# Kernel optimization log

Measured on AMD Instinct MI355X. Metric: run time of the kernel, lower is better.

## Reference

```python
import jax, jax.numpy as jnp
import numpy as np

EMBED_DIM = 768
N_HEADS = 12
HEAD_DIM = EMBED_DIM // N_HEADS
SCALE = HEAD_DIM ** 0.5


def setup_inputs() -> dict:
    key = jax.random.key(0)
    k1, k2, k3 = jax.random.split(key, 3)
    x = jax.random.normal(k1, (2, 2048, EMBED_DIM), dtype=jnp.float32)
    # weights stored [in, out] so forward is x @ W (equivalent to torch Linear with W.T)
    w_qkv = jax.random.normal(k2, (EMBED_DIM, 3 * EMBED_DIM), dtype=jnp.float32) * (EMBED_DIM ** -0.5)
    w_proj = jax.random.normal(k3, (EMBED_DIM, EMBED_DIM), dtype=jnp.float32) * (EMBED_DIM ** -0.5)
    return {"x": x, "w_qkv": w_qkv, "w_proj": w_proj}


def reference(x, w_qkv, w_proj):
    B, N, C = x.shape
    qkv = x @ w_qkv  # [B, N, 3C]
    qkv = qkv.reshape(B, N, 3, N_HEADS, HEAD_DIM)
    qkv = jnp.transpose(qkv, (2, 0, 3, 1, 4))  # [3, B, H, N, hd]
    q, k, v = qkv[0], qkv[1], qkv[2]
    attn = jnp.einsum("bhnd,bhmd->bhnm", q, k) / SCALE  # [B, H, N, N]
    attn = jax.nn.softmax(attn, axis=-1)
    out = jnp.einsum("bhnm,bhmd->bhnd", attn, v)  # [B, H, N, hd]
    out = jnp.transpose(out, (0, 2, 1, 3)).reshape(B, N, C)
    return out @ w_proj
```

## Files before the change

kernel.cpp:

```cpp
#include <hip/hip_runtime.h>
#include <hip/hip_bf16.h>
#include <stdint.h>

typedef uint16_t u16;
typedef __attribute__((ext_vector_type(4))) float f32x4;
typedef __attribute__((ext_vector_type(8))) short bf16x8;

#define LOG2E 1.4426950408889634f

static __device__ __forceinline__ u16 f2b(float x){
  union { float f; uint32_t u; } a; a.f = x;
  uint32_t r = a.u + 0x7FFFu + ((a.u >> 16) & 1u);
  return (u16)(r >> 16);
}

static __device__ __forceinline__ uint32_t pkrhu(float lo, float hi){
  union { float f; uint32_t u; } a, b; a.f = lo; b.f = hi;
  return __builtin_amdgcn_perm(b.u + 0x8000u, a.u + 0x8000u, 0x07060302u);
}

#define GLD16(g, l) __builtin_amdgcn_global_load_lds((const __attribute__((address_space(1))) void*)(g), (__attribute__((address_space(3))) void*)(l), 16, 0, 0)

__global__ __launch_bounds__(256) void k_prep(const float* __restrict__ x, u16* __restrict__ Xb,
                                              const float* __restrict__ wqkv, u16* __restrict__ WqkvT,
                                              const float* __restrict__ wproj, u16* __restrict__ WprojT){
  __shared__ float t[32][33];
  const int bid = blockIdx.x, tid = threadIdx.x;
  if (bid < 1536){
    int i = bid * 256 + tid;
    const f32x4* p = (const f32x4*)(x + (size_t)i * 8);
    f32x4 a = p[0], b = p[1];
    u16 h[8];
#pragma unroll
    for (int j = 0; j < 4; ++j){ h[j] = f2b(a[j]); h[4+j] = f2b(b[j]); }
    *(bf16x8*)(Xb + (size_t)i * 8) = *(const bf16x8*)h;
    return;
  }
  const float* in; u16* out; int R, C, bx, by;
  if (bid < 1536 + 1728){
    int q = bid - 1536; in = wqkv; out = WqkvT; R = 768; C = 2304; bx = q % 72; by = q / 72;
  } else {
    int q = bid - 1536 - 1728; in = wproj; out = WprojT; R = 768; C = 768; bx = q % 24; by = q / 24;
  }
  int c0 = bx * 32, r0 = by * 32;
  int tx = tid & 31, ty = tid >> 5;
#pragma unroll
  for (int i = 0; i < 32; i += 8) t[ty + i][tx] = in[(size_t)(r0 + ty + i) * C + c0 + tx];
  __syncthreads();
#pragma unroll
  for (int i = 0; i < 32; i += 8) out[(size_t)(c0 + ty + i) * R + r0 + tx] = f2b(t[tx][ty + i]);
}

__global__ __launch_bounds__(256) void k_gemmqkv(const u16* __restrict__ A, const u16* __restrict__ Bt,
                                                 u16* __restrict__ Qp, u16* __restrict__ Kp, u16* __restrict__ Vtp){
  __shared__ __align__(16) u16 SM[14336];
  u16* Al = SM; u16* Bl = SM + 8192;
  const int tid = threadIdx.x;
  const int w = tid >> 6, l = tid & 63;
  const int m0 = blockIdx.x * 128, n0 = blockIdx.y * 96;
  const int wm = (w >> 1) * 64, wn = (w & 1) * 48;
  const int lg = l >> 4, lr = l & 15;
  f32x4 acc[4][3] = {};
  const u16* asrc = A  + (size_t)(m0 + w*32 + (l >> 3)) * 768 + (l & 7) * 8;
  const u16* bsrc = Bt + (size_t)(n0 + w*24 + (l >> 3)) * 768 + (l & 7) * 8;
  for (int k0 = 0; k0 < 768; k0 += 64){
#pragma unroll
    for (int i = 0; i < 4; ++i)
      GLD16(asrc + (size_t)(i*8)*768 + k0, &Al[(w*32 + i*8) * 64]);
#pragma unroll
    for (int i = 0; i < 3; ++i)
      GLD16(bsrc + (size_t)(i*8)*768 + k0, &Bl[(w*24 + i*8) * 64]);
    __syncthreads();
    bf16x8 af[4][2], bfr[3][2];
#pragma unroll
    for (int mf = 0; mf < 4; ++mf)
#pragma unroll
      for (int ks = 0; ks < 2; ++ks)
        af[mf][ks] = *(const bf16x8*)&Al[(wm + mf*16 + lr) * 64 + ks*32 + lg*8];
#pragma unroll
    for (int nf = 0; nf < 3; ++nf)
#pragma unroll
      for (int ks = 0; ks < 2; ++ks)
        bfr[nf][ks] = *(const bf16x8*)&Bl[(wn + nf*16 + lr) * 64 + ks*32 + lg*8];
#pragma unroll
    for (int ks = 0; ks < 2; ++ks)
#pragma unroll
      for (int mf = 0; mf < 4; ++mf)
#pragma unroll
        for (int nf = 0; nf < 3; ++nf)
          acc[mf][nf] = __builtin_amdgcn_mfma_f32_16x16x32_bf16(af[mf][ks], bfr[nf][ks], acc[mf][nf], 0, 0, 0);
    __syncthreads();
  }

  const int which = n0 / 768;
  const int nl0 = n0 - which * 768;
  if (which < 2){
    u16* dst = (which == 0) ? Qp : Kp;
    const float sc = (which == 0) ? 0.125f * LOG2E : 1.0f;
#pragma unroll
    for (int mf = 0; mf < 4; ++mf)
#pragma unroll
      for (int nf = 0; nf < 3; ++nf)
#pragma unroll
        for (int r = 0; r < 4; ++r){
          int m = m0 + wm + mf*16 + lg*4 + r;
          int n = nl0 + wn + nf*16 + lr;
          int b = m >> 11, row = m & 2047, hh = n >> 6, d = n & 63;
          dst[(size_t)((b*12 + hh)*2048 + row) * 64 + d] = f2b(acc[mf][nf][r] * sc);
        }
  } else {
#pragma unroll
    for (int mf = 0; mf < 4; ++mf)
#pragma unroll
      for (int nf = 0; nf < 3; ++nf)
#pragma unroll
        for (int r = 0; r < 4; ++r){
          int mrow = wm + mf*16 + lg*4 + r;
          int c    = wn + nf*16 + lr;
          SM[c * 128 + mrow] = f2b(acc[mf][nf][r]);
        }
    __syncthreads();
#pragma unroll
    for (int rr = 0; rr < 6; ++rr){
      int c  = rr*16 + (tid >> 4);
      int mo = (tid & 15) * 8;
      bf16x8 v = *(const bf16x8*)&SM[c * 128 + mo];
      int n = nl0 + c, hh = n >> 6, d = n & 63;
      int m = m0 + mo, b = m >> 11, key = m & 2047;
      *(bf16x8*)&Vtp[(size_t)((b*12 + hh)*64 + d) * 2048 + key] = v;
    }
  }
}

__global__ __launch_bounds__(256) void k_gemm64(const u16* __restrict__ A, const u16* __restrict__ Bt,
                                                float* __restrict__ Co){
  __shared__ __align__(16) u16 SM[8192];
  u16* Al = SM; u16* Bl = SM + 4096;
  const int tid = threadIdx.x;
  const int w = tid >> 6, l = tid & 63;
  const int m0 = blockIdx.x * 64, n0 = blockIdx.y * 64;
  const int wm = (w >> 1) * 32, wn = (w & 1) * 32;
  const int lg = l >> 4, lr = l & 15;
  f32x4 acc[2][2] = {};
  const u16* asrc = A  + (size_t)(m0 + w*16 + (l >> 3)) * 768 + (l & 7) * 8;
  const u16* bsrc = Bt + (size_t)(n0 + w*16 + (l >> 3)) * 768 + (l & 7) * 8;
  for (int k0 = 0; k0 < 768; k0 += 64){
#pragma unroll
    for (int i = 0; i < 2; ++i){
      GLD16(asrc + (size_t)(i*8)*768 + k0, &Al[(w*16 + i*8) * 64]);
      GLD16(bsrc + (size_t)(i*8)*768 + k0, &Bl[(w*16 + i*8) * 64]);
    }
    __syncthreads();
    bf16x8 af[2][2], bfr[2][2];
#pragma unroll
    for (int mf = 0; mf < 2; ++mf)
#pragma unroll
      for (int ks = 0; ks < 2; ++ks){
        af[mf][ks]  = *(const bf16x8*)&Al[(wm + mf*16 + lr) * 64 + ks*32 + lg*8];
        bfr[mf][ks] = *(const bf16x8*)&Bl[(wn + mf*16 + lr) * 64 + ks*32 + lg*8];
      }
#pragma unroll
    for (int ks = 0; ks < 2; ++ks)
#pragma unroll
      for (int mf = 0; mf < 2; ++mf)
#pragma unroll
        for (int nf = 0; nf < 2; ++nf)
          acc[mf][nf] = __builtin_amdgcn_mfma_f32_16x16x32_bf16(af[mf][ks], bfr[nf][ks], acc[mf][nf], 0, 0, 0);
    __syncthreads();
  }
#pragma unroll
  for (int mf = 0; mf < 2; ++mf)
#pragma unroll
    for (int nf = 0; nf < 2; ++nf)
#pragma unroll
      for (int r = 0; r < 4; ++r)
        Co[(size_t)(m0 + wm + mf*16 + lg*4 + r) * 768 + n0 + wn + nf*16 + lr] = acc[mf][nf][r];
}

__global__ __launch_bounds__(256) void k_attn(const u16* __restrict__ Qp, const u16* __restrict__ Kp,
                                              const u16* __restrict__ Vtp, u16* __restrict__ AO){
  __shared__ __align__(16) u16 SM[24576];
  const int tid = threadIdx.x, w = tid >> 6, l = tid & 63;
  const int qh = w >> 1, kh = w & 1;
  const int lg = l >> 4, lr = l & 15;
  const int qt_b = blockIdx.x, bh = blockIdx.y;
  const int b = bh / 12, hh = bh - b * 12;
  const size_t base = (size_t)bh * (2048 * 64);
  const u16* Qg = Qp + base; const u16* Kg = Kp + base; const u16* Vg = Vtp + base;
  const int q0w = qt_b * 64 + qh * 32;
  const int rsw = (lr & 7) * 8;

  bf16x8 qf[2][2];
#pragma unroll
  for (int qt = 0; qt < 2; ++qt)
#pragma unroll
    for (int ks = 0; ks < 2; ++ks)
      qf[qt][ks] = *(const bf16x8*)&Qg[(size_t)(q0w + qt*16 + lr) * 64 + ks*32 + lg*8];

  f32x4 oacc[2][4] = {};
  float lp[2] = {0.f, 0.f};

  const int pl0 = w*8 + (l >> 3);
  const int sk0 = 8*((pl0 >> 2) & 3) + 4*((pl0 >> 4) & 1) + (pl0 & 3);
  const int csw = (((l & 7) ^ ((l >> 3) & 7)) << 3);
  const u16* kLp = Kg + (size_t)sk0 * 64 + csw;
  const u16* kUp = kLp + 32 * 64;
  const u16* vLp = Vg + ((size_t)pl0 << 11) + csw;
  const u16* vUp = vLp + ((size_t)32 << 11);
  const int dlo = (w*8) * 64, dhi = (w*8 + 32) * 64;
  u16* const K0lo = SM + 0     + dlo;  u16* const K0hi = SM + 0     + dhi;
  u16* const K1lo = SM + 4096  + dlo;  u16* const K1hi = SM + 4096  + dhi;
  u16* const K2lo = SM + 8192  + dlo;  u16* const K2hi = SM + 8192  + dhi;
  u16* const V0lo = SM + 12288 + dlo;  u16* const V0hi = SM + 12288 + dhi;
  u16* const V1lo = SM + 16384 + dlo;  u16* const V1hi = SM + 16384 + dhi;
  u16* const V2lo = SM + 20480 + dlo;  u16* const V2hi = SM + 20480 + dhi;

  auto compute = [&](const u16* Kc, const u16* Vc){
    f32x4 s[2][2] = {};
    bf16x8 kfr[2][2];
#pragma unroll
    for (int kf = 0; kf < 2; ++kf)
#pragma unroll
      for (int ks = 0; ks < 2; ++ks)
        kfr[kf][ks] = *(const bf16x8*)&Kc[(kh*32 + kf*16 + lr) * 64 + ((ks*32 + lg*8) ^ rsw)];
    __builtin_amdgcn_s_setprio(1);
#pragma unroll
    for (int ks = 0; ks < 2; ++ks)
#pragma unroll
      for (int kf = 0; kf < 2; ++kf)
#pragma unroll
        for (int qt = 0; qt < 2; ++qt)
          s[qt][kf] = __builtin_amdgcn_mfma_f32_16x16x32_bf16(kfr[kf][ks], qf[qt][ks], s[qt][kf], 0, 0, 0);
    __builtin_amdgcn_s_setprio(0);

    bf16x8 pa[2];
#pragma unroll
    for (int qt = 0; qt < 2; ++qt){
      float p00 = __builtin_exp2f(s[qt][0][0]);
      float p01 = __builtin_exp2f(s[qt][0][1]);
      float p02 = __builtin_exp2f(s[qt][0][2]);
      float p03 = __builtin_exp2f(s[qt][0][3]);
      float p10 = __builtin_exp2f(s[qt][1][0]);
      float p11 = __builtin_exp2f(s[qt][1][1]);
      float p12 = __builtin_exp2f(s[qt][1][2]);
      float p13 = __builtin_exp2f(s[qt][1][3]);
      lp[qt] += ((p00 + p01) + (p02 + p03)) + ((p10 + p11) + (p12 + p13));
      union { uint32_t u[4]; bf16x8 v; } fr;
      fr.u[0] = pkrhu(p00, p01);
      fr.u[1] = pkrhu(p02, p03);
      fr.u[2] = pkrhu(p10, p11);
      fr.u[3] = pkrhu(p12, p13);
      pa[qt] = fr.v;
    }

    bf16x8 vfr[4];
#pragma unroll
    for (int nf = 0; nf < 4; ++nf)
      vfr[nf] = *(const bf16x8*)&Vc[(nf*16 + lr) * 64 + ((kh*32 + lg*8) ^ rsw)];
    __builtin_amdgcn_s_setprio(1);
#pragma unroll
    for (int qt = 0; qt < 2; ++qt)
#pragma unroll
      for (int nf = 0; nf < 4; ++nf)
        oacc[qt][nf] = __builtin_amdgcn_mfma_f32_16x16x32_bf16(vfr[nf], pa[qt], oacc[qt][nf], 0, 0, 0);
    __builtin_amdgcn_s_setprio(0);
  };

#define STAGE4(KL, KH, VL, VH) do { GLD16(kLp, KL); GLD16(kUp, KH); GLD16(vLp, VL); GLD16(vUp, VH); \
                                    kLp += 4096; kUp += 4096; vLp += 64; vUp += 64; } while(0)
#define BAR_CNT8  do { asm volatile("s_waitcnt vmcnt(8)" ::: "memory"); \
                       __builtin_amdgcn_s_barrier(); __builtin_amdgcn_sched_barrier(0); } while(0)
#define BAR_CNT0  do { asm volatile("s_waitcnt vmcnt(0)" ::: "memory"); \
                       __builtin_amdgcn_s_barrier(); __builtin_amdgcn_sched_barrier(0); } while(0)

  STAGE4(K0lo, K0hi, V0lo, V0hi);
  STAGE4(K1lo, K1hi, V1lo, V1hi);
  BAR_CNT8;

  for (int g = 0; g < 10; ++g){
    STAGE4(K2lo, K2hi, V2lo, V2hi);
    compute(SM + 0,     SM + 12288);
    BAR_CNT8;
    STAGE4(K0lo, K0hi, V0lo, V0hi);
    compute(SM + 4096,  SM + 16384);
    BAR_CNT8;
    STAGE4(K1lo, K1hi, V1lo, V1hi);
    compute(SM + 8192,  SM + 20480);
    BAR_CNT8;
  }
  compute(SM + 0,    SM + 12288);
  BAR_CNT0;
  compute(SM + 4096, SM + 16384);

#undef STAGE4
#undef BAR_CNT8
#undef BAR_CNT0

  float lt[2];
#pragma unroll
  for (int qt = 0; qt < 2; ++qt){
    float t = lp[qt];
    t += __shfl_xor(t, 16);
    t += __shfl_xor(t, 32);
    lt[qt] = t;
  }

  __syncthreads();
  float* Osc = (float*)SM;
  float* Lsc = Osc + 64 * 65;
  if (kh == 1){
#pragma unroll
    for (int qt = 0; qt < 2; ++qt)
#pragma unroll
      for (int nf = 0; nf < 4; ++nf)
#pragma unroll
        for (int r = 0; r < 4; ++r)
          Osc[(qh*32 + qt*16 + lr) * 65 + nf*16 + lg*4 + r] = oacc[qt][nf][r];
    if (lg == 0){
      Lsc[qh*32 + lr]      = lt[0];
      Lsc[qh*32 + 16 + lr] = lt[1];
    }
  }
  __syncthreads();
  if (kh == 0){
#pragma unroll
    for (int qt = 0; qt < 2; ++qt){
      float inv = 1.0f / (lt[qt] + Lsc[qh*32 + qt*16 + lr]);
#pragma unroll
      for (int nf = 0; nf < 4; ++nf)
#pragma unroll
        for (int r = 0; r < 4; ++r){
          float o = oacc[qt][nf][r] + Osc[(qh*32 + qt*16 + lr) * 65 + nf*16 + lg*4 + r];
          AO[(size_t)((b << 11) + q0w + qt*16 + lr) * 768 + hh*64 + nf*16 + lg*4 + r] = f2b(o * inv);
        }
    }
  }
}

extern "C" void kernel_launch(void* const* d_in, const int* in_sizes, int n_in,
                              void* d_out, int out_size, void* d_ws, size_t ws_size,
                              hipStream_t stream){
  const float* x      = (const float*)d_in[0];
  const float* w_qkv  = (const float*)d_in[1];
  const float* w_proj = (const float*)d_in[2];
  float* out = (float*)d_out;
  char* ws = (char*)d_ws;
  u16* Xb     = (u16*)(ws + 0);
  u16* WqkvT  = (u16*)(ws + 6291456);
  u16* WprojT = (u16*)(ws + 9830400);
  u16* Qp     = (u16*)(ws + 11010048);
  u16* Kp     = (u16*)(ws + 17301504);
  u16* Vtp    = (u16*)(ws + 23592960);
  u16* AO     = (u16*)(ws + 29884416);

  k_prep<<<3840, 256, 0, stream>>>(x, Xb, w_qkv, WqkvT, w_proj, WprojT);
  k_gemmqkv<<<dim3(32, 24), 256, 0, stream>>>(Xb, WqkvT, Qp, Kp, Vtp);
  k_attn<<<dim3(32, 24), 256, 0, stream>>>(Qp, Kp, Vtp, AO);
  k_gemm64<<<dim3(64, 12), 256, 0, stream>>>(AO, WprojT, out);
}
```

Baseline: 91.41 us.

## Double attention block to 512 threads with 16-row query tiles per wave

The attention kernel now runs 8 waves per block instead of 4, and each wave owns a 16-row query tile instead of two, which halves per-wave accumulator state. The 64-key tile loads are spread across all 512 threads with two async LDS loads each, and the wait count is adjusted to match. Launch bounds request 6 blocks per CU. The aim is more waves in flight to hide latency, paid for with less reuse of each K/V fragment read from LDS per MFMA, since every K/V fragment is now read by twice as many waves.

```diff
diff --git a/kernel.cpp b/kernel.cpp
--- a/kernel.cpp
+++ b/kernel.cpp
@@ -177,163 +177,128 @@
         Co[(size_t)(m0 + wm + mf*16 + lg*4 + r) * 768 + n0 + wn + nf*16 + lr] = acc[mf][nf][r];
 }
 
-__global__ __launch_bounds__(256) void k_attn(const u16* __restrict__ Qp, const u16* __restrict__ Kp,
-                                              const u16* __restrict__ Vtp, u16* __restrict__ AO){
+__global__ __launch_bounds__(512, 6) void k_attn(const u16* __restrict__ Qp, const u16* __restrict__ Kp,
+                                                 const u16* __restrict__ Vtp, u16* __restrict__ AO){
   __shared__ __align__(16) u16 SM[24576];
   const int tid = threadIdx.x, w = tid >> 6, l = tid & 63;
-  const int qh = w >> 1, kh = w & 1;
+  const int qh = w >> 2, kh = (w >> 1) & 1;
+  const int QH = w >> 1, KH = w & 1;
   const int lg = l >> 4, lr = l & 15;
   const int qt_b = blockIdx.x, bh = blockIdx.y;
   const int b = bh / 12, hh = bh - b * 12;
   const size_t base = (size_t)bh * (2048 * 64);
   const u16* Qg = Qp + base; const u16* Kg = Kp + base; const u16* Vg = Vtp + base;
-  const int q0w = qt_b * 64 + qh * 32;
+  const int q0w = qt_b * 64 + QH * 16;
   const int rsw = (lr & 7) * 8;
 
-  bf16x8 qf[2][2];
-#pragma unroll
-  for (int qt = 0; qt < 2; ++qt)
+  bf16x8 qf[2];
+#pragma unroll
+  for (int ks = 0; ks < 2; ++ks)
+    qf[ks] = *(const bf16x8*)&Qg[(size_t)(q0w + lr) * 64 + ks*32 + lg*8];
+
+  f32x4 oacc[4] = {};
+  float lp = 0.f;
+
+  const int p_  = tid >> 3;
+  const int sk  = 32*(p_ >> 5) + 8*((p_ >> 2) & 3) + 4*((p_ >> 4) & 1) + (p_ & 3);
+  const int cs8 = (((tid & 7) ^ (p_ & 7)) << 3);
+  const u16* kp = Kg + (size_t)sk * 64 + cs8;
+  const u16* vp = Vg + ((size_t)p_ << 11) + cs8;
+  const int drow = p_ * 64;
+  u16* const K0 = SM + 0     + drow;  u16* const V0 = SM + 12288 + drow;
+  u16* const K1 = SM + 4096  + drow;  u16* const V1 = SM + 16384 + drow;
+  u16* const K2 = SM + 8192  + drow;  u16* const V2 = SM + 20480 + drow;
+
+  auto compute = [&](const u16* Kc, const u16* Vc){
+    f32x4 s[2] = {};
+    bf16x8 kfr[2][2];
+#pragma unroll
+    for (int kf = 0; kf < 2; ++kf)
+#pragma unroll
+      for (int ks = 0; ks < 2; ++ks)
+        kfr[kf][ks] = *(const bf16x8*)&Kc[(KH*32 + kf*16 + lr) * 64 + ((ks*32 + lg*8) ^ rsw)];
+    __builtin_amdgcn_s_setprio(1);
 #pragma unroll
     for (int ks = 0; ks < 2; ++ks)
-      qf[qt][ks] = *(const bf16x8*)&Qg[(size_t)(q0w + qt*16 + lr) * 64 + ks*32 + lg*8];
-
-  f32x4 oacc[2][4] = {};
-  float lp[2] = {0.f, 0.f};
-
-  const int pl0 = w*8 + (l >> 3);
-  const int sk0 = 8*((pl0 >> 2) & 3) + 4*((pl0 >> 4) & 1) + (pl0 & 3);
-  const int csw = (((l & 7) ^ ((l >> 3) & 7)) << 3);
-  const u16* kLp = Kg + (size_t)sk0 * 64 + csw;
-  const u16* kUp = kLp + 32 * 64;
-  const u16* vLp = Vg + ((size_t)pl0 << 11) + csw;
-  const u16* vUp = vLp + ((size_t)32 << 11);
-  const int dlo = (w*8) * 64, dhi = (w*8 + 32) * 64;
-  u16* const K0lo = SM + 0     + dlo;  u16* const K0hi = SM + 0     + dhi;
-  u16* const K1lo = SM + 4096  + dlo;  u16* const K1hi = SM + 4096  + dhi;
-  u16* const K2lo = SM + 8192  + dlo;  u16* const K2hi = SM + 8192  + dhi;
-  u16* const V0lo = SM + 12288 + dlo;  u16* const V0hi = SM + 12288 + dhi;
-  u16* const V1lo = SM + 16384 + dlo;  u16* const V1hi = SM + 16384 + dhi;
-  u16* const V2lo = SM + 20480 + dlo;  u16* const V2hi = SM + 20480 + dhi;
-
-  auto compute = [&](const u16* Kc, const u16* Vc){
-    f32x4 s[2][2] = {};
-    bf16x8 kfr[2][2];
-#pragma unroll
-    for (int kf = 0; kf < 2; ++kf)
-#pragma unroll
-      for (int ks = 0; ks < 2; ++ks)
-        kfr[kf][ks] = *(const bf16x8*)&Kc[(kh*32 + kf*16 + lr) * 64 + ((ks*32 + lg*8) ^ rsw)];
+#pragma unroll
+      for (int kf = 0; kf < 2; ++kf)
+        s[kf] = __builtin_amdgcn_mfma_f32_16x16x32_bf16(kfr[kf][ks], qf[ks], s[kf], 0, 0, 0);
+    __builtin_amdgcn_s_setprio(0);
+
+    float p00 = __builtin_exp2f(s[0][0]);
+    float p01 = __builtin_exp2f(s[0][1]);
+    float p02 = __builtin_exp2f(s[0][2]);
+    float p03 = __builtin_exp2f(s[0][3]);
+    float p10 = __builtin_exp2f(s[1][0]);
+    float p11 = __builtin_exp2f(s[1][1]);
+    float p12 = __builtin_exp2f(s[1][2]);
+    float p13 = __builtin_exp2f(s[1][3]);
+    lp += ((p00 + p01) + (p02 + p03)) + ((p10 + p11) + (p12 + p13));
+    union { uint32_t u[4]; bf16x8 v; } fr;
+    fr.u[0] = pkrhu(p00, p01);
+    fr.u[1] = pkrhu(p02, p03);
+    fr.u[2] = pkrhu(p10, p11);
+    fr.u[3] = pkrhu(p12, p13);
+
+    bf16x8 vfr[4];
+#pragma unroll
+    for (int nf = 0; nf < 4; ++nf)
+      vfr[nf] = *(const bf16x8*)&Vc[(nf*16 + lr) * 64 + ((KH*32 + lg*8) ^ rsw)];
     __builtin_amdgcn_s_setprio(1);
 #pragma unroll
-    for (int ks = 0; ks < 2; ++ks)
-#pragma unroll
-      for (int kf = 0; kf < 2; ++kf)
-#pragma unroll
-        for (int qt = 0; qt < 2; ++qt)
-          s[qt][kf] = __builtin_amdgcn_mfma_f32_16x16x32_bf16(kfr[kf][ks], qf[qt][ks], s[qt][kf], 0, 0, 0);
-    __builtin_amdgcn_s_setprio(0);
-
-    bf16x8 pa[2];
-#pragma unroll
-    for (int qt = 0; qt < 2; ++qt){
-      float p00 = __builtin_exp2f(s[qt][0][0]);
-      float p01 = __builtin_exp2f(s[qt][0][1]);
-      float p02 = __builtin_exp2f(s[qt][0][2]);
-      float p03 = __builtin_exp2f(s[qt][0][3]);
-      float p10 = __builtin_exp2f(s[qt][1][0]);
-      float p11 = __builtin_exp2f(s[qt][1][1]);
-      float p12 = __builtin_exp2f(s[qt][1][2]);
-      float p13 = __builtin_exp2f(s[qt][1][3]);
-      lp[qt] += ((p00 + p01) + (p02 + p03)) + ((p10 + p11) + (p12 + p13));
-      union { uint32_t u[4]; bf16x8 v; } fr;
-      fr.u[0] = pkrhu(p00, p01);
-      fr.u[1] = pkrhu(p02, p03);
-      fr.u[2] = pkrhu(p10, p11);
-      fr.u[3] = pkrhu(p12, p13);
-      pa[qt] = fr.v;
-    }
-
-    bf16x8 vfr[4];
-#pragma unroll
     for (int nf = 0; nf < 4; ++nf)
-      vfr[nf] = *(const bf16x8*)&Vc[(nf*16 + lr) * 64 + ((kh*32 + lg*8) ^ rsw)];
-    __builtin_amdgcn_s_setprio(1);
-#pragma unroll
-    for (int qt = 0; qt < 2; ++qt)
-#pragma unroll
-      for (int nf = 0; nf < 4; ++nf)
-        oacc[qt][nf] = __builtin_amdgcn_mfma_f32_16x16x32_bf16(vfr[nf], pa[qt], oacc[qt][nf], 0, 0, 0);
+      oacc[nf] = __builtin_amdgcn_mfma_f32_16x16x32_bf16(vfr[nf], fr.v, oacc[nf], 0, 0, 0);
     __builtin_amdgcn_s_setprio(0);
   };
 
-#define STAGE4(KL, KH, VL, VH) do { GLD16(kLp, KL); GLD16(kUp, KH); GLD16(vLp, VL); GLD16(vUp, VH); \
-                                    kLp += 4096; kUp += 4096; vLp += 64; vUp += 64; } while(0)
-#define BAR_CNT8  do { asm volatile("s_waitcnt vmcnt(8)" ::: "memory"); \
+#define STAGE2(KD, VD) do { GLD16(kp, KD); GLD16(vp, VD); kp += 4096; vp += 64; } while(0)
+#define BAR_CNT2  do { asm volatile("s_waitcnt vmcnt(2)" ::: "memory"); \
                        __builtin_amdgcn_s_barrier(); __builtin_amdgcn_sched_barrier(0); } while(0)
 #define BAR_CNT0  do { asm volatile("s_waitcnt vmcnt(0)" ::: "memory"); \
                        __builtin_amdgcn_s_barrier(); __builtin_amdgcn_sched_barrier(0); } while(0)
 
-  STAGE4(K0lo, K0hi, V0lo, V0hi);
-  STAGE4(K1lo, K1hi, V1lo, V1hi);
-  BAR_CNT8;
+  STAGE2(K0, V0);
+  STAGE2(K1, V1);
+  BAR_CNT2;
 
   for (int g = 0; g < 10; ++g){
-    STAGE4(K2lo, K2hi, V2lo, V2hi);
-    compute(SM + 0,     SM + 12288);
-    BAR_CNT8;
-    STAGE4(K0lo, K0hi, V0lo, V0hi);
-    compute(SM + 4096,  SM + 16384);
-    BAR_CNT8;
-    STAGE4(K1lo, K1hi, V1lo, V1hi);
-    compute(SM + 8192,  SM + 20480);
-    BAR_CNT8;
+    STAGE2(K2, V2);  compute(SM + 0,    SM + 12288);  BAR_CNT2;
+    STAGE2(K0, V0);  compute(SM + 4096, SM + 16384);  BAR_CNT2;
+    STAGE2(K1, V1);  compute(SM + 8192, SM + 20480);  BAR_CNT2;
   }
   compute(SM + 0,    SM + 12288);
   BAR_CNT0;
   compute(SM + 4096, SM + 16384);
 
-#undef STAGE4
-#undef BAR_CNT8
+#undef STAGE2
+#undef BAR_CNT2
 #undef BAR_CNT0
 
-  float lt[2];
-#pragma unroll
-  for (int qt = 0; qt < 2; ++qt){
-    float t = lp[qt];
-    t += __shfl_xor(t, 16);
-    t += __shfl_xor(t, 32);
-    lt[qt] = t;
-  }
+  float lt = lp;
+  lt += __shfl_xor(lt, 16);
+  lt += __shfl_xor(lt, 32);
 
   __syncthreads();
   float* Osc = (float*)SM;
   float* Lsc = Osc + 64 * 65;
-  if (kh == 1){
-#pragma unroll
-    for (int qt = 0; qt < 2; ++qt)
-#pragma unroll
-      for (int nf = 0; nf < 4; ++nf)
-#pragma unroll
-        for (int r = 0; r < 4; ++r)
-          Osc[(qh*32 + qt*16 + lr) * 65 + nf*16 + lg*4 + r] = oacc[qt][nf][r];
-    if (lg == 0){
-      Lsc[qh*32 + lr]      = lt[0];
-      Lsc[qh*32 + 16 + lr] = lt[1];
-    }
+  if (KH == 1){
+#pragma unroll
+    for (int nf = 0; nf < 4; ++nf)
+#pragma unroll
+      for (int r = 0; r < 4; ++r)
+        Osc[(QH*16 + lr) * 65 + nf*16 + lg*4 + r] = oacc[nf][r];
+    if (lg == 0) Lsc[QH*16 + lr] = lt;
   }
   __syncthreads();
-  if (kh == 0){
-#pragma unroll
-    for (int qt = 0; qt < 2; ++qt){
-      float inv = 1.0f / (lt[qt] + Lsc[qh*32 + qt*16 + lr]);
-#pragma unroll
-      for (int nf = 0; nf < 4; ++nf)
-#pragma unroll
-        for (int r = 0; r < 4; ++r){
-          float o = oacc[qt][nf][r] + Osc[(qh*32 + qt*16 + lr) * 65 + nf*16 + lg*4 + r];
-          AO[(size_t)((b << 11) + q0w + qt*16 + lr) * 768 + hh*64 + nf*16 + lg*4 + r] = f2b(o * inv);
-        }
-    }
+  if (KH == 0){
+    float inv = 1.0f / (lt + Lsc[QH*16 + lr]);
+#pragma unroll
+    for (int nf = 0; nf < 4; ++nf)
+#pragma unroll
+      for (int r = 0; r < 4; ++r){
+        float o = oacc[nf][r] + Osc[(QH*16 + lr) * 65 + nf*16 + lg*4 + r];
+        AO[(size_t)((b << 11) + q0w + lr) * 768 + hh*64 + nf*16 + lg*4 + r] = f2b(o * inv);
+      }
   }
 }
 
@@ -355,6 +320,6 @@
 
   k_prep<<<3840, 256, 0, stream>>>(x, Xb, w_qkv, WqkvT, w_proj, WprojT);
   k_gemmqkv<<<dim3(32, 24), 256, 0, stream>>>(Xb, WqkvT, Qp, Kp, Vtp);
-  k_attn<<<dim3(32, 24), 256, 0, stream>>>(Qp, Kp, Vtp, AO);
+  k_attn<<<dim3(32, 24), 512, 0, stream>>>(Qp, Kp, Vtp, AO);
   k_gemm64<<<dim3(64, 12), 256, 0, stream>>>(AO, WprojT, out);
 }
```

Result: faster. 88.46 us (-3.2%).
